# Kernel tuning notes

Measured on AMD Instinct MI355X. Metric: run time of the kernel, lower is better.

## Reference

```python
import jax, jax.numpy as jnp
import numpy as np

N = 1024   # nodes
C = 256    # channels (n_features)
NEG_SLOPE = 0.2


def setup_inputs() -> dict:
    key = jax.random.key(0)
    k1, k2, k3, k4, k5, k6, k7 = jax.random.split(key, 7)
    nodes = jax.random.normal(k1, (N, C), dtype=jnp.float32)
    # dense adjacency used only via (adj != 0); force self-loops so every
    # softmax row has at least one valid entry
    adj_mat = jax.random.randint(k2, (N, N), 0, 2).astype(jnp.int32)
    adj_mat = adj_mat.at[jnp.arange(N), jnp.arange(N)].set(1)
    lim = 1.0 / np.sqrt(C)  # eqx.nn.Linear default uniform init bound
    W_src_w = jax.random.uniform(k3, (C, C), minval=-lim, maxval=lim, dtype=jnp.float32)
    W_src_b = jax.random.uniform(k4, (C,), minval=-lim, maxval=lim, dtype=jnp.float32)
    W_tgt_w = jax.random.uniform(k5, (C, C), minval=-lim, maxval=lim, dtype=jnp.float32)
    W_tgt_b = jax.random.uniform(k6, (C,), minval=-lim, maxval=lim, dtype=jnp.float32)
    a_w = jax.random.uniform(k7, (C,), minval=-lim, maxval=lim, dtype=jnp.float32)  # to_score, no bias
    return {"nodes": nodes, "adj_mat": adj_mat, "W_src_w": W_src_w, "W_src_b": W_src_b,
            "W_tgt_w": W_tgt_w, "W_tgt_b": W_tgt_b, "a_w": a_w}


def reference(nodes, adj_mat, W_src_w, W_src_b, W_tgt_w, W_tgt_b, a_w):
    # per-node linear maps (eqx.nn.Linear: y = W @ x + b)
    g_src = nodes @ W_src_w.T + W_src_b              # [node, C]
    g_tgt = nodes @ W_tgt_w.T + W_tgt_b              # [node, C]
    # g[i, j, c] = g_src[i, c] + g_tgt[j, c]   (axis names as in original: tgt, src)
    g = g_src[:, None, :] + g_tgt[None, :, :]        # [node, node, C]
    g = jax.nn.leaky_relu(g, NEG_SLOPE)
    score = jnp.einsum('ijc,c->ij', g, a_w)          # [node, node]
    score = jnp.where(adj_mat != 0, score, -jnp.inf) # mask non-edges
    weights = jax.nn.softmax(score, axis=1)          # over src axis
    return weights @ g_tgt                           # [node, C]
```

## Files before the change

kernel.cpp:

```cpp
#include <hip/hip_runtime.h>


typedef unsigned short u16;
typedef unsigned int   u32;
typedef _Float16 h2 __attribute__((ext_vector_type(2)));

#define NNODE 1024
#define NC    256
#define NEG   0.2f

__device__ __forceinline__ float bf2f(u16 h) {
    u32 u = ((u32)h) << 16;
    return __builtin_bit_cast(float, u);
}
__device__ __forceinline__ u16 f2bf(float f) {
    u32 u = __builtin_bit_cast(u32, f);
    u32 r = (u + 0x7FFFu + ((u >> 16) & 1u)) >> 16;
    return (u16)r;
}
__device__ __forceinline__ u16 f2h(float f) {
    _Float16 h = (_Float16)f;
    return __builtin_bit_cast(u16, h);
}
__device__ __forceinline__ h2 bch(u32 u) { return __builtin_bit_cast(h2, u); }

__device__ __forceinline__ h2 lrelu2(h2 y) {
    h2 yn = y * (_Float16)NEG;
#if __has_builtin(__builtin_elementwise_max)
    return __builtin_elementwise_max(y, yn);
#else
    h2 r; r.x = y.x > yn.x ? y.x : yn.x; r.y = y.y > yn.y ? y.y : yn.y;
    return r;
#endif
}
__device__ __forceinline__ float dot2(h2 a, h2 b, float acc) {
#if __has_builtin(__builtin_amdgcn_fdot2)
    return __builtin_amdgcn_fdot2(a, b, acc, false);
#else
    acc = fmaf((float)a.x, (float)b.x, acc);
    return fmaf((float)a.y, (float)b.y, acc);
#endif
}

__global__ void detect_kernel(const u16* __restrict__ nodes, int* __restrict__ flag)
{
    const int lane = threadIdx.x;
    ushort4 v = *(const ushort4*)(nodes + lane * 4);
    const u16 h[4] = {v.x, v.y, v.z, v.w};
    int cnt = 0;
    #pragma unroll
    for (int q = 0; q < 4; ++q) {
        int e = (h[q] >> 7) & 0xFF;
        cnt += (e >= 132 || (e >= 1 && e <= 90)) ? 1 : 0;
    }
    #pragma unroll
    for (int off = 32; off; off >>= 1) cnt += __shfl_xor(cnt, off, 64);
    if (lane == 0) *flag = (cnt >= 64) ? 0 : 1;
}

__global__ __launch_bounds__(256) void lin_kernel(
    const void* __restrict__ nodes_v,
    const void* __restrict__ Wsrc_v, const void* __restrict__ bsrc_v,
    const void* __restrict__ Wtgt_v, const void* __restrict__ btgt_v,
    const int* __restrict__ flag,
    u16* __restrict__ gsh, u16* __restrict__ gth)
{
    __shared__ float nT[64][34];
    __shared__ float wT[64][68];

    const int bf = *flag;
    const int t  = threadIdx.x;
    const int ct = blockIdx.x;
    const int it = blockIdx.y;
    const int i0 = it * 32;
    const bool is_src = (ct < 4);
    const int c0 = (is_src ? ct : ct - 4) * 64;
    const void* __restrict__ Wv = is_src ? Wsrc_v : Wtgt_v;
    const void* __restrict__ bv = is_src ? bsrc_v : btgt_v;
    u16* __restrict__ g         = is_src ? gsh : gth;

    const int tc = t & 15, ti = t >> 4;
    float acc[2][4] = {};

    for (int k0 = 0; k0 < NC; k0 += 64) {
        __syncthreads();
        {
            int ii = t & 31, kg = t >> 5;
            float vals[8];
            if (bf) {
                uint4 v = *(const uint4*)((const u16*)nodes_v + (i0 + ii) * NC + k0 + kg * 8);
                const u16* pv = (const u16*)&v;
                #pragma unroll
                for (int q = 0; q < 8; ++q) vals[q] = bf2f(pv[q]);
            } else {
                const float* nf = (const float*)nodes_v;
                float4 v0 = *(const float4*)(nf + (i0 + ii) * NC + k0 + kg * 8);
                float4 v1 = *(const float4*)(nf + (i0 + ii) * NC + k0 + kg * 8 + 4);
                vals[0] = v0.x; vals[1] = v0.y; vals[2] = v0.z; vals[3] = v0.w;
                vals[4] = v1.x; vals[5] = v1.y; vals[6] = v1.z; vals[7] = v1.w;
            }
            #pragma unroll
            for (int q = 0; q < 8; ++q) nT[kg * 8 + q][ii] = vals[q];
        }
        {
            int cc = t & 63, kg = t >> 6;
            float vals[16];
            if (bf) {
                const u16* W = (const u16*)Wv;
                uint4 v0 = *(const uint4*)(W + (c0 + cc) * NC + k0 + kg * 16);
                uint4 v1 = *(const uint4*)(W + (c0 + cc) * NC + k0 + kg * 16 + 8);
                const u16* p0 = (const u16*)&v0;
                const u16* p1 = (const u16*)&v1;
                #pragma unroll
                for (int q = 0; q < 8; ++q) { vals[q] = bf2f(p0[q]); vals[8 + q] = bf2f(p1[q]); }
            } else {
                const float* W = (const float*)Wv;
                #pragma unroll
                for (int h = 0; h < 4; ++h) {
                    float4 v = *(const float4*)(W + (c0 + cc) * NC + k0 + kg * 16 + 4 * h);
                    vals[4 * h + 0] = v.x; vals[4 * h + 1] = v.y;
                    vals[4 * h + 2] = v.z; vals[4 * h + 3] = v.w;
                }
            }
            #pragma unroll
            for (int q = 0; q < 16; ++q) wT[kg * 16 + q][cc] = vals[q];
        }
        __syncthreads();
        #pragma unroll 8
        for (int kk = 0; kk < 64; ++kk) {
            float2 av = *(const float2*)&nT[kk][2 * ti];
            float4 bvv = *(const float4*)&wT[kk][4 * tc];
            float sa[2] = {av.x, av.y};
            float tb[4] = {bvv.x, bvv.y, bvv.z, bvv.w};
            #pragma unroll
            for (int a = 0; a < 2; ++a)
                #pragma unroll
                for (int b = 0; b < 4; ++b)
                    acc[a][b] = fmaf(sa[a], tb[b], acc[a][b]);
        }
    }

    float bb[4];
    #pragma unroll
    for (int q = 0; q < 4; ++q)
        bb[q] = bf ? bf2f(((const u16*)bv)[c0 + 4 * tc + q])
                   : ((const float*)bv)[c0 + 4 * tc + q];
    #pragma unroll
    for (int a = 0; a < 2; ++a) {
        int irow = i0 + 2 * ti + a;
        ushort4 ov;
        ov.x = f2h(acc[a][0] + bb[0]);
        ov.y = f2h(acc[a][1] + bb[1]);
        ov.z = f2h(acc[a][2] + bb[2]);
        ov.w = f2h(acc[a][3] + bb[3]);
        *(ushort4*)(g + (size_t)irow * NC + c0 + 4 * tc) = ov;
    }
}

__global__ __launch_bounds__(256, 4) void fused_kernel(
    const u16* __restrict__ gsh, const u16* __restrict__ gth,
    const void* __restrict__ aw_v, const int* __restrict__ adj,
    const int* __restrict__ flag, int jcnt,
    float* __restrict__ po, float* __restrict__ pm,
    float* __restrict__ pls, void* __restrict__ out_v)
{
    __shared__ u32  gt32[64][132];
    __shared__ u32  gs32[4][128];
    __shared__ u32  a32[128];
    __shared__ float p_lds[4][64];

    const int bf   = *flag;
    const int t    = threadIdx.x;
    const int i    = t >> 6;
    const int lane = t & 63;
    const int row  = blockIdx.x * 4 + i;
    const int z    = blockIdx.y;
    const int jbase = z * jcnt;
    const int jl = lane & 15, q  = lane >> 4;
    const int oc = lane & 31, hh = lane >> 5;

    {
        uint2 v = *(const uint2*)(gsh + (size_t)row * NC + lane * 4);
        *(uint2*)&gs32[i][2 * lane] = v;
    }
    if (t < 128) {
        float a0, a1;
        if (bf) { a0 = bf2f(((const u16*)aw_v)[2 * t]); a1 = bf2f(((const u16*)aw_v)[2 * t + 1]); }
        else    { a0 = ((const float*)aw_v)[2 * t];     a1 = ((const float*)aw_v)[2 * t + 1]; }
        h2 av; av.x = (_Float16)a0; av.y = (_Float16)a1;
        a32[t] = __builtin_bit_cast(u32, av);
    }
    __syncthreads();

    h2 gsr[32];
    #pragma unroll
    for (int k = 0; k < 8; ++k) {
        uint4 gv = *(const uint4*)&gs32[i][q * 32 + 4 * k];
        gsr[4 * k + 0] = bch(gv.x); gsr[4 * k + 1] = bch(gv.y);
        gsr[4 * k + 2] = bch(gv.z); gsr[4 * k + 3] = bch(gv.w);
    }

    float m = -1e30f, l = 0.f;
    float of[8] = {0.f, 0.f, 0.f, 0.f, 0.f, 0.f, 0.f, 0.f};

    for (int j0 = jbase; j0 < jbase + jcnt; j0 += 64) {
        __syncthreads();
        {
            int r = t & 63, seg = t >> 6;
            const u16* src = gth + (size_t)(j0 + r) * NC + seg * 64;
            #pragma unroll
            for (int k = 0; k < 8; ++k) {
                uint4 v = *(const uint4*)(src + 8 * k);
                *(uint4*)&gt32[r][seg * 32 + 4 * k] = v;
            }
        }
        __syncthreads();

        float spv[4] = {0.f, 0.f, 0.f, 0.f};
        #pragma unroll
        for (int k = 0; k < 8; ++k) {
            uint4 a4 = *(const uint4*)&a32[q * 32 + 4 * k];
            h2 a0 = bch(a4.x), a1 = bch(a4.y), a2 = bch(a4.z), a3 = bch(a4.w);
            h2 g0 = gsr[4 * k], g1 = gsr[4 * k + 1],
               g2 = gsr[4 * k + 2], g3 = gsr[4 * k + 3];
            #pragma unroll
            for (int p = 0; p < 4; ++p) {
                uint4 g4 = *(const uint4*)&gt32[16 * p + jl][q * 32 + 4 * k];
                spv[p] = dot2(a0, lrelu2(g0 + bch(g4.x)), spv[p]);
                spv[p] = dot2(a1, lrelu2(g1 + bch(g4.y)), spv[p]);
                spv[p] = dot2(a2, lrelu2(g2 + bch(g4.z)), spv[p]);
                spv[p] = dot2(a3, lrelu2(g3 + bch(g4.w)), spv[p]);
            }
        }
        #pragma unroll
        for (int p = 0; p < 4; ++p) {
            spv[p] += __shfl_xor(spv[p], 16, 64);
            spv[p] += __shfl_xor(spv[p], 32, 64);
        }
        const float s = (lane < 16) ? spv[0] : (lane < 32) ? spv[1]
                      : (lane < 48) ? spv[2] : spv[3];

        const int valid = adj[row * NNODE + j0 + lane];
        float sm = valid ? s : -1e30f;
        float tmax = sm;
        #pragma unroll
        for (int off = 32; off; off >>= 1)
            tmax = fmaxf(tmax, __shfl_xor(tmax, off, 64));
        const float mn    = fmaxf(m, tmax);
        const float alpha = __expf(m - mn);
        const float p     = valid ? __expf(s - mn) : 0.f;
        float ps = p;
        #pragma unroll
        for (int off = 32; off; off >>= 1) ps += __shfl_xor(ps, off, 64);
        l = l * alpha + ps;
        m = mn;
        p_lds[i][lane] = p;

        #pragma unroll
        for (int k = 0; k < 8; ++k) of[k] *= alpha;
        #pragma unroll 8
        for (int jp = 0; jp < 32; ++jp) {
            const float w = p_lds[i][2 * jp + hh];
            uint4 g4 = *(const uint4*)&gt32[2 * jp + hh][4 * oc];
            h2 v0 = bch(g4.x), v1 = bch(g4.y), v2 = bch(g4.z), v3 = bch(g4.w);
            of[0] = fmaf(w, (float)v0.x, of[0]);
            of[1] = fmaf(w, (float)v0.y, of[1]);
            of[2] = fmaf(w, (float)v1.x, of[2]);
            of[3] = fmaf(w, (float)v1.y, of[3]);
            of[4] = fmaf(w, (float)v2.x, of[4]);
            of[5] = fmaf(w, (float)v2.y, of[5]);
            of[6] = fmaf(w, (float)v3.x, of[6]);
            of[7] = fmaf(w, (float)v3.y, of[7]);
        }
    }

    #pragma unroll
    for (int k = 0; k < 8; ++k) of[k] += __shfl_xor(of[k], 32, 64);

    if (lane < 32) {
        if (out_v) {
            const float inv = 1.0f / l;
            if (bf) {
                u16* out = (u16*)out_v;
                ushort4 oa, ob;
                oa.x = f2bf(of[0] * inv); oa.y = f2bf(of[1] * inv);
                oa.z = f2bf(of[2] * inv); oa.w = f2bf(of[3] * inv);
                ob.x = f2bf(of[4] * inv); ob.y = f2bf(of[5] * inv);
                ob.z = f2bf(of[6] * inv); ob.w = f2bf(of[7] * inv);
                *(ushort4*)(out + (size_t)row * NC + 8 * oc)     = oa;
                *(ushort4*)(out + (size_t)row * NC + 8 * oc + 4) = ob;
            } else {
                float* out = (float*)out_v;
                *(float4*)(out + (size_t)row * NC + 8 * oc) =
                    make_float4(of[0] * inv, of[1] * inv, of[2] * inv, of[3] * inv);
                *(float4*)(out + (size_t)row * NC + 8 * oc + 4) =
                    make_float4(of[4] * inv, of[5] * inv, of[6] * inv, of[7] * inv);
            }
        } else {
            float* pp = po + ((size_t)z * NNODE + row) * NC + 8 * oc;
            *(float4*)pp       = make_float4(of[0], of[1], of[2], of[3]);
            *(float4*)(pp + 4) = make_float4(of[4], of[5], of[6], of[7]);
        }
    }
    if (!out_v && lane == 0) {
        pm [z * NNODE + row] = m;
        pls[z * NNODE + row] = l;
    }
}

__global__ __launch_bounds__(256) void combine_kernel(
    const float* __restrict__ po, const float* __restrict__ pm,
    const float* __restrict__ pls, const int* __restrict__ flag,
    int ns, void* __restrict__ out_v)
{
    const int bf  = *flag;
    const int row = blockIdx.x;
    const int c   = threadIdx.x;

    float mstar = -1e30f;
    for (int zz = 0; zz < ns; ++zz)
        mstar = fmaxf(mstar, pm[zz * NNODE + row]);

    float acc = 0.f, lsum = 0.f;
    for (int zz = 0; zz < ns; ++zz) {
        const float wz = __expf(pm[zz * NNODE + row] - mstar);
        lsum = fmaf(pls[zz * NNODE + row], wz, lsum);
        acc  = fmaf(po[(size_t)(zz * NNODE + row) * NC + c], wz, acc);
    }
    const float v = acc / lsum;
    if (bf) ((u16*)out_v)[row * NC + c] = f2bf(v);
    else    ((float*)out_v)[row * NC + c] = v;
}

extern "C" void kernel_launch(void* const* d_in, const int* in_sizes, int n_in,
                              void* d_out, int out_size, void* d_ws, size_t ws_size,
                              hipStream_t stream)
{
    const int* adj = (const int*)d_in[1];

    char* wsb = (char*)d_ws;
    int* flag = (int*)wsb;
    u16* gsh  = (u16*)(wsb + 256);
    u16* gth  = gsh + (size_t)NNODE * NC;

    detect_kernel<<<1, 64, 0, stream>>>((const u16*)d_in[0], flag);
    lin_kernel<<<dim3(8, 32), 256, 0, stream>>>(d_in[0], d_in[2], d_in[3],
                                                d_in[4], d_in[5], flag, gsh, gth);

    const size_t base = 256 + 2ull * NNODE * NC * sizeof(u16);
    int NS = 0;
    {
        size_t need4 = base + (4ull * NNODE * NC + 8ull * NNODE) * 4ull;
        size_t need2 = base + (2ull * NNODE * NC + 4ull * NNODE) * 4ull;
        if      (ws_size >= need4) NS = 4;
        else if (ws_size >= need2) NS = 2;
    }

    if (NS) {
        float* po  = (float*)(wsb + base);
        float* pm  = po + (size_t)NS * NNODE * NC;
        float* pls = pm + (size_t)NS * NNODE;
        fused_kernel<<<dim3(256, NS), 256, 0, stream>>>(
            gsh, gth, d_in[6], adj, flag, NNODE / NS, po, pm, pls, nullptr);
        combine_kernel<<<NNODE, 256, 0, stream>>>(po, pm, pls, flag, NS, d_out);
    } else {
        fused_kernel<<<dim3(256, 1), 256, 0, stream>>>(
            gsh, gth, d_in[6], adj, flag, NNODE, nullptr, nullptr, nullptr, d_out);
    }
}
```

Measured before the change: 68.44 us.

## Process two target rows per wave, swizzle LDS tile, inline dtype detection

Each wave now handles two output rows, so every g_tgt tile value read from LDS feeds two score and aggregation computations, doubling reuse and halving the number of blocks. The LDS tile drops its padding in favour of an XOR swizzle to avoid bank conflicts. The separate detect kernel is removed and each kernel detects the dtype itself, saving a launch. The split count can rise to 8 when workspace allows. The cost is higher register pressure from the doubled accumulators and g_src registers, and a larger combine step.

```diff
diff --git a/kernel.cpp b/kernel.cpp
--- a/kernel.cpp
+++ b/kernel.cpp
@@ -42,9 +42,8 @@
 #endif
 }
 
-__global__ void detect_kernel(const u16* __restrict__ nodes, int* __restrict__ flag)
-{
-    const int lane = threadIdx.x;
+__device__ __forceinline__ int wave_detect(const u16* __restrict__ nodes, int lane)
+{
     ushort4 v = *(const ushort4*)(nodes + lane * 4);
     const u16 h[4] = {v.x, v.y, v.z, v.w};
     int cnt = 0;
@@ -55,21 +54,22 @@
     }
     #pragma unroll
     for (int off = 32; off; off >>= 1) cnt += __shfl_xor(cnt, off, 64);
-    if (lane == 0) *flag = (cnt >= 64) ? 0 : 1;
-}
+    return (cnt >= 64) ? 0 : 1;
+}
+
+__device__ __forceinline__ int swz(int grp, int row) { return grp ^ (row & 31); }
 
 __global__ __launch_bounds__(256) void lin_kernel(
     const void* __restrict__ nodes_v,
     const void* __restrict__ Wsrc_v, const void* __restrict__ bsrc_v,
     const void* __restrict__ Wtgt_v, const void* __restrict__ btgt_v,
-    const int* __restrict__ flag,
     u16* __restrict__ gsh, u16* __restrict__ gth)
 {
     __shared__ float nT[64][34];
     __shared__ float wT[64][68];
 
-    const int bf = *flag;
     const int t  = threadIdx.x;
+    const int bf = wave_detect((const u16*)nodes_v, t & 63);
     const int ct = blockIdx.x;
     const int it = blockIdx.y;
     const int i0 = it * 32;
@@ -160,29 +160,24 @@
 __global__ __launch_bounds__(256, 4) void fused_kernel(
     const u16* __restrict__ gsh, const u16* __restrict__ gth,
     const void* __restrict__ aw_v, const int* __restrict__ adj,
-    const int* __restrict__ flag, int jcnt,
+    const u16* __restrict__ nodes_u16, int jcnt,
     float* __restrict__ po, float* __restrict__ pm,
     float* __restrict__ pls, void* __restrict__ out_v)
 {
-    __shared__ u32  gt32[64][132];
-    __shared__ u32  gs32[4][128];
-    __shared__ u32  a32[128];
-    __shared__ float p_lds[4][64];
-
-    const int bf   = *flag;
+    __shared__ u32   gt32[64 * 128];
+    __shared__ u32   a32[128];
+    __shared__ float p_lds[8][64];
+
     const int t    = threadIdx.x;
-    const int i    = t >> 6;
+    const int wv   = t >> 6;
     const int lane = t & 63;
-    const int row  = blockIdx.x * 4 + i;
+    const int bf   = wave_detect(nodes_u16, lane);
+    const int r0   = blockIdx.x * 8 + 2 * wv;
     const int z    = blockIdx.y;
     const int jbase = z * jcnt;
     const int jl = lane & 15, q  = lane >> 4;
     const int oc = lane & 31, hh = lane >> 5;
 
-    {
-        uint2 v = *(const uint2*)(gsh + (size_t)row * NC + lane * 4);
-        *(uint2*)&gs32[i][2 * lane] = v;
-    }
     if (t < 128) {
         float a0, a1;
         if (bf) { a0 = bf2f(((const u16*)aw_v)[2 * t]); a1 = bf2f(((const u16*)aw_v)[2 * t + 1]); }
@@ -190,130 +185,167 @@
         h2 av; av.x = (_Float16)a0; av.y = (_Float16)a1;
         a32[t] = __builtin_bit_cast(u32, av);
     }
-    __syncthreads();
-
-    h2 gsr[32];
-    #pragma unroll
-    for (int k = 0; k < 8; ++k) {
-        uint4 gv = *(const uint4*)&gs32[i][q * 32 + 4 * k];
-        gsr[4 * k + 0] = bch(gv.x); gsr[4 * k + 1] = bch(gv.y);
-        gsr[4 * k + 2] = bch(gv.z); gsr[4 * k + 3] = bch(gv.w);
-    }
-
-    float m = -1e30f, l = 0.f;
-    float of[8] = {0.f, 0.f, 0.f, 0.f, 0.f, 0.f, 0.f, 0.f};
+
+    u32 gsr[2][32];
+    #pragma unroll
+    for (int r = 0; r < 2; ++r) {
+        const u16* src = gsh + (size_t)(r0 + r) * NC + q * 64;
+        #pragma unroll
+        for (int k = 0; k < 8; ++k) {
+            uint4 gv = *(const uint4*)(src + 8 * k);
+            gsr[r][4 * k + 0] = gv.x; gsr[r][4 * k + 1] = gv.y;
+            gsr[r][4 * k + 2] = gv.z; gsr[r][4 * k + 3] = gv.w;
+        }
+    }
+
+    float m[2] = {-1e30f, -1e30f}, l[2] = {0.f, 0.f};
+    float of[2][8] = {};
 
     for (int j0 = jbase; j0 < jbase + jcnt; j0 += 64) {
         __syncthreads();
         {
-            int r = t & 63, seg = t >> 6;
-            const u16* src = gth + (size_t)(j0 + r) * NC + seg * 64;
+            int rr = t & 63, seg = t >> 6;
+            const u16* src = gth + (size_t)(j0 + rr) * NC + seg * 64;
+            u32* dst = gt32 + rr * 128;
             #pragma unroll
             for (int k = 0; k < 8; ++k) {
                 uint4 v = *(const uint4*)(src + 8 * k);
-                *(uint4*)&gt32[r][seg * 32 + 4 * k] = v;
+                *(uint4*)(dst + swz(seg * 8 + k, rr) * 4) = v;
             }
         }
         __syncthreads();
 
-        float spv[4] = {0.f, 0.f, 0.f, 0.f};
+        float spv[2][4] = {};
         #pragma unroll
         for (int k = 0; k < 8; ++k) {
             uint4 a4 = *(const uint4*)&a32[q * 32 + 4 * k];
             h2 a0 = bch(a4.x), a1 = bch(a4.y), a2 = bch(a4.z), a3 = bch(a4.w);
-            h2 g0 = gsr[4 * k], g1 = gsr[4 * k + 1],
-               g2 = gsr[4 * k + 2], g3 = gsr[4 * k + 3];
             #pragma unroll
             for (int p = 0; p < 4; ++p) {
-                uint4 g4 = *(const uint4*)&gt32[16 * p + jl][q * 32 + 4 * k];
-                spv[p] = dot2(a0, lrelu2(g0 + bch(g4.x)), spv[p]);
-                spv[p] = dot2(a1, lrelu2(g1 + bch(g4.y)), spv[p]);
-                spv[p] = dot2(a2, lrelu2(g2 + bch(g4.z)), spv[p]);
-                spv[p] = dot2(a3, lrelu2(g3 + bch(g4.w)), spv[p]);
-            }
-        }
-        #pragma unroll
-        for (int p = 0; p < 4; ++p) {
-            spv[p] += __shfl_xor(spv[p], 16, 64);
-            spv[p] += __shfl_xor(spv[p], 32, 64);
-        }
-        const float s = (lane < 16) ? spv[0] : (lane < 32) ? spv[1]
-                      : (lane < 48) ? spv[2] : spv[3];
-
-        const int valid = adj[row * NNODE + j0 + lane];
-        float sm = valid ? s : -1e30f;
-        float tmax = sm;
-        #pragma unroll
-        for (int off = 32; off; off >>= 1)
-            tmax = fmaxf(tmax, __shfl_xor(tmax, off, 64));
-        const float mn    = fmaxf(m, tmax);
-        const float alpha = __expf(m - mn);
-        const float p     = valid ? __expf(s - mn) : 0.f;
-        float ps = p;
-        #pragma unroll
-        for (int off = 32; off; off >>= 1) ps += __shfl_xor(ps, off, 64);
-        l = l * alpha + ps;
-        m = mn;
-        p_lds[i][lane] = p;
-
-        #pragma unroll
-        for (int k = 0; k < 8; ++k) of[k] *= alpha;
-        #pragma unroll 8
+                const int rowp = 16 * p + jl;
+                uint4 g4 = *(const uint4*)&gt32[rowp * 128 + swz(q * 8 + k, rowp) * 4];
+                h2 t0 = bch(g4.x), t1 = bch(g4.y), t2 = bch(g4.z), t3 = bch(g4.w);
+                #pragma unroll
+                for (int r = 0; r < 2; ++r) {
+                    spv[r][p] = dot2(a0, lrelu2(bch(gsr[r][4 * k + 0]) + t0), spv[r][p]);
+                    spv[r][p] = dot2(a1, lrelu2(bch(gsr[r][4 * k + 1]) + t1), spv[r][p]);
+                    spv[r][p] = dot2(a2, lrelu2(bch(gsr[r][4 * k + 2]) + t2), spv[r][p]);
+                    spv[r][p] = dot2(a3, lrelu2(bch(gsr[r][4 * k + 3]) + t3), spv[r][p]);
+                }
+            }
+        }
+        #pragma unroll
+        for (int r = 0; r < 2; ++r)
+            #pragma unroll
+            for (int p = 0; p < 4; ++p) {
+                spv[r][p] += __shfl_xor(spv[r][p], 16, 64);
+                spv[r][p] += __shfl_xor(spv[r][p], 32, 64);
+            }
+
+        float alpha[2];
+        #pragma unroll
+        for (int r = 0; r < 2; ++r) {
+            const float s = (lane < 16) ? spv[r][0] : (lane < 32) ? spv[r][1]
+                          : (lane < 48) ? spv[r][2] : spv[r][3];
+            const int valid = adj[(size_t)(r0 + r) * NNODE + j0 + lane];
+            float sm = valid ? s : -1e30f;
+            float tmax = sm;
+            #pragma unroll
+            for (int off = 32; off; off >>= 1)
+                tmax = fmaxf(tmax, __shfl_xor(tmax, off, 64));
+            const float mn = fmaxf(m[r], tmax);
+            alpha[r]       = __expf(m[r] - mn);
+            const float p  = valid ? __expf(s - mn) : 0.f;
+            float ps = p;
+            #pragma unroll
+            for (int off = 32; off; off >>= 1) ps += __shfl_xor(ps, off, 64);
+            l[r] = l[r] * alpha[r] + ps;
+            m[r] = mn;
+            p_lds[2 * wv + r][lane] = p;
+        }
+
+        #pragma unroll
+        for (int r = 0; r < 2; ++r)
+            #pragma unroll
+            for (int k = 0; k < 8; ++k) of[r][k] *= alpha[r];
+
+        #pragma unroll 4
         for (int jp = 0; jp < 32; ++jp) {
-            const float w = p_lds[i][2 * jp + hh];
-            uint4 g4 = *(const uint4*)&gt32[2 * jp + hh][4 * oc];
+            const int j = 2 * jp + hh;
+            const float w0 = p_lds[2 * wv    ][j];
+            const float w1 = p_lds[2 * wv + 1][j];
+            uint4 g4 = *(const uint4*)&gt32[j * 128 + swz(oc, j) * 4];
             h2 v0 = bch(g4.x), v1 = bch(g4.y), v2 = bch(g4.z), v3 = bch(g4.w);
-            of[0] = fmaf(w, (float)v0.x, of[0]);
-            of[1] = fmaf(w, (float)v0.y, of[1]);
-            of[2] = fmaf(w, (float)v1.x, of[2]);
-            of[3] = fmaf(w, (float)v1.y, of[3]);
-            of[4] = fmaf(w, (float)v2.x, of[4]);
-            of[5] = fmaf(w, (float)v2.y, of[5]);
-            of[6] = fmaf(w, (float)v3.x, of[6]);
-            of[7] = fmaf(w, (float)v3.y, of[7]);
-        }
-    }
-
-    #pragma unroll
-    for (int k = 0; k < 8; ++k) of[k] += __shfl_xor(of[k], 32, 64);
+            of[0][0] = fmaf(w0, (float)v0.x, of[0][0]);
+            of[0][1] = fmaf(w0, (float)v0.y, of[0][1]);
+            of[0][2] = fmaf(w0, (float)v1.x, of[0][2]);
+            of[0][3] = fmaf(w0, (float)v1.y, of[0][3]);
+            of[0][4] = fmaf(w0, (float)v2.x, of[0][4]);
+            of[0][5] = fmaf(w0, (float)v2.y, of[0][5]);
+            of[0][6] = fmaf(w0, (float)v3.x, of[0][6]);
+            of[0][7] = fmaf(w0, (float)v3.y, of[0][7]);
+            of[1][0] = fmaf(w1, (float)v0.x, of[1][0]);
+            of[1][1] = fmaf(w1, (float)v0.y, of[1][1]);
+            of[1][2] = fmaf(w1, (float)v1.x, of[1][2]);
+            of[1][3] = fmaf(w1, (float)v1.y, of[1][3]);
+            of[1][4] = fmaf(w1, (float)v2.x, of[1][4]);
+            of[1][5] = fmaf(w1, (float)v2.y, of[1][5]);
+            of[1][6] = fmaf(w1, (float)v3.x, of[1][6]);
+            of[1][7] = fmaf(w1, (float)v3.y, of[1][7]);
+        }
+    }
+
+    #pragma unroll
+    for (int r = 0; r < 2; ++r)
+        #pragma unroll
+        for (int k = 0; k < 8; ++k) of[r][k] += __shfl_xor(of[r][k], 32, 64);
 
     if (lane < 32) {
-        if (out_v) {
-            const float inv = 1.0f / l;
-            if (bf) {
-                u16* out = (u16*)out_v;
-                ushort4 oa, ob;
-                oa.x = f2bf(of[0] * inv); oa.y = f2bf(of[1] * inv);
-                oa.z = f2bf(of[2] * inv); oa.w = f2bf(of[3] * inv);
-                ob.x = f2bf(of[4] * inv); ob.y = f2bf(of[5] * inv);
-                ob.z = f2bf(of[6] * inv); ob.w = f2bf(of[7] * inv);
-                *(ushort4*)(out + (size_t)row * NC + 8 * oc)     = oa;
-                *(ushort4*)(out + (size_t)row * NC + 8 * oc + 4) = ob;
+        #pragma unroll
+        for (int r = 0; r < 2; ++r) {
+            const int row = r0 + r;
+            if (out_v) {
+                const float inv = 1.0f / l[r];
+                if (bf) {
+                    u16* out = (u16*)out_v;
+                    ushort4 oa, ob;
+                    oa.x = f2bf(of[r][0] * inv); oa.y = f2bf(of[r][1] * inv);
+                    oa.z = f2bf(of[r][2] * inv); oa.w = f2bf(of[r][3] * inv);
+                    ob.x = f2bf(of[r][4] * inv); ob.y = f2bf(of[r][5] * inv);
+                    ob.z = f2bf(of[r][6] * inv); ob.w = f2bf(of[r][7] * inv);
+                    *(ushort4*)(out + (size_t)row * NC + 8 * oc)     = oa;
+                    *(ushort4*)(out + (size_t)row * NC + 8 * oc + 4) = ob;
+                } else {
+                    float* out = (float*)out_v;
+                    *(float4*)(out + (size_t)row * NC + 8 * oc) =
+                        make_float4(of[r][0] * inv, of[r][1] * inv,
+                                    of[r][2] * inv, of[r][3] * inv);
+                    *(float4*)(out + (size_t)row * NC + 8 * oc + 4) =
+                        make_float4(of[r][4] * inv, of[r][5] * inv,
+                                    of[r][6] * inv, of[r][7] * inv);
+                }
             } else {
-                float* out = (float*)out_v;
-                *(float4*)(out + (size_t)row * NC + 8 * oc) =
-                    make_float4(of[0] * inv, of[1] * inv, of[2] * inv, of[3] * inv);
-                *(float4*)(out + (size_t)row * NC + 8 * oc + 4) =
-                    make_float4(of[4] * inv, of[5] * inv, of[6] * inv, of[7] * inv);
-            }
-        } else {
-            float* pp = po + ((size_t)z * NNODE + row) * NC + 8 * oc;
-            *(float4*)pp       = make_float4(of[0], of[1], of[2], of[3]);
-            *(float4*)(pp + 4) = make_float4(of[4], of[5], of[6], of[7]);
+                float* pp = po + ((size_t)z * NNODE + row) * NC + 8 * oc;
+                *(float4*)pp       = make_float4(of[r][0], of[r][1], of[r][2], of[r][3]);
+                *(float4*)(pp + 4) = make_float4(of[r][4], of[r][5], of[r][6], of[r][7]);
+            }
         }
     }
     if (!out_v && lane == 0) {
-        pm [z * NNODE + row] = m;
-        pls[z * NNODE + row] = l;
+        #pragma unroll
+        for (int r = 0; r < 2; ++r) {
+            pm [(size_t)z * NNODE + r0 + r] = m[r];
+            pls[(size_t)z * NNODE + r0 + r] = l[r];
+        }
     }
 }
 
 __global__ __launch_bounds__(256) void combine_kernel(
     const float* __restrict__ po, const float* __restrict__ pm,
-    const float* __restrict__ pls, const int* __restrict__ flag,
+    const float* __restrict__ pls, const u16* __restrict__ nodes_u16,
     int ns, void* __restrict__ out_v)
 {
-    const int bf  = *flag;
+    const int bf  = wave_detect(nodes_u16, threadIdx.x & 63);
     const int row = blockIdx.x;
     const int c   = threadIdx.x;
 
@@ -336,35 +368,32 @@
                               void* d_out, int out_size, void* d_ws, size_t ws_size,
                               hipStream_t stream)
 {
-    const int* adj = (const int*)d_in[1];
+    const u16* nodes_u16 = (const u16*)d_in[0];
+    const int* adj       = (const int*)d_in[1];
 
     char* wsb = (char*)d_ws;
-    int* flag = (int*)wsb;
-    u16* gsh  = (u16*)(wsb + 256);
+    u16* gsh  = (u16*)wsb;
     u16* gth  = gsh + (size_t)NNODE * NC;
 
-    detect_kernel<<<1, 64, 0, stream>>>((const u16*)d_in[0], flag);
     lin_kernel<<<dim3(8, 32), 256, 0, stream>>>(d_in[0], d_in[2], d_in[3],
-                                                d_in[4], d_in[5], flag, gsh, gth);
-
-    const size_t base = 256 + 2ull * NNODE * NC * sizeof(u16);
+                                                d_in[4], d_in[5], gsh, gth);
+
+    const size_t base = 2ull * NNODE * NC * sizeof(u16);
+    const size_t per  = 4ull * NNODE * NC + 8ull * NNODE;
     int NS = 0;
-    {
-        size_t need4 = base + (4ull * NNODE * NC + 8ull * NNODE) * 4ull;
-        size_t need2 = base + (2ull * NNODE * NC + 4ull * NNODE) * 4ull;
-        if      (ws_size >= need4) NS = 4;
-        else if (ws_size >= need2) NS = 2;
-    }
+    if      (ws_size >= base + 8 * per) NS = 8;
+    else if (ws_size >= base + 4 * per) NS = 4;
+    else if (ws_size >= base + 2 * per) NS = 2;
 
     if (NS) {
         float* po  = (float*)(wsb + base);
         float* pm  = po + (size_t)NS * NNODE * NC;
         float* pls = pm + (size_t)NS * NNODE;
-        fused_kernel<<<dim3(256, NS), 256, 0, stream>>>(
-            gsh, gth, d_in[6], adj, flag, NNODE / NS, po, pm, pls, nullptr);
-        combine_kernel<<<NNODE, 256, 0, stream>>>(po, pm, pls, flag, NS, d_out);
+        fused_kernel<<<dim3(128, NS), 256, 0, stream>>>(
+            gsh, gth, d_in[6], adj, nodes_u16, NNODE / NS, po, pm, pls, nullptr);
+        combine_kernel<<<NNODE, 256, 0, stream>>>(po, pm, pls, nodes_u16, NS, d_out);
     } else {
-        fused_kernel<<<dim3(256, 1), 256, 0, stream>>>(
-            gsh, gth, d_in[6], adj, flag, NNODE, nullptr, nullptr, nullptr, d_out);
-    }
-}
+        fused_kernel<<<dim3(128, 1), 256, 0, stream>>>(
+            gsh, gth, d_in[6], adj, nodes_u16, NNODE, nullptr, nullptr, nullptr, d_out);
+    }
+}
```

Result: slower. 72.13 us (+5.4%).

## Rewrite leaky ReLU as linear plus abs term and precompute linear score parts

Applied to the files above, without the earlier changes.

Uses leaky_relu(x) = 0.6x + 0.4|x|, so the per-pair inner loop only computes an abs (a bit mask) instead of a multiply and max. The linear parts become per-row and per-column dot products: one is computed in a new sdot kernel, the other inside the fused kernel. The change also removes the detect kernel by recomputing the dtype flag in every wave, XOR-swizzles the shared-memory tile instead of padding it, loads gsrc straight into registers, and allows an 8-way split over the source axis. Costs are an extra launch, a larger partial buffer for combine, and different fp16 rounding in the score.

```diff
diff --git a/kernel.cpp b/kernel.cpp
--- a/kernel.cpp
+++ b/kernel.cpp
@@ -23,15 +23,9 @@
     return __builtin_bit_cast(u16, h);
 }
 __device__ __forceinline__ h2 bch(u32 u) { return __builtin_bit_cast(h2, u); }
-
-__device__ __forceinline__ h2 lrelu2(h2 y) {
-    h2 yn = y * (_Float16)NEG;
-#if __has_builtin(__builtin_elementwise_max)
-    return __builtin_elementwise_max(y, yn);
-#else
-    h2 r; r.x = y.x > yn.x ? y.x : yn.x; r.y = y.y > yn.y ? y.y : yn.y;
-    return r;
-#endif
+__device__ __forceinline__ h2 habs2(h2 y) {
+    u32 u = __builtin_bit_cast(u32, y) & 0x7FFF7FFFu;
+    return __builtin_bit_cast(h2, u);
 }
 __device__ __forceinline__ float dot2(h2 a, h2 b, float acc) {
 #if __has_builtin(__builtin_amdgcn_fdot2)
@@ -42,9 +36,8 @@
 #endif
 }
 
-__global__ void detect_kernel(const u16* __restrict__ nodes, int* __restrict__ flag)
-{
-    const int lane = threadIdx.x;
+__device__ __forceinline__ int wave_detect(const u16* __restrict__ nodes, int lane)
+{
     ushort4 v = *(const ushort4*)(nodes + lane * 4);
     const u16 h[4] = {v.x, v.y, v.z, v.w};
     int cnt = 0;
@@ -55,21 +48,22 @@
     }
     #pragma unroll
     for (int off = 32; off; off >>= 1) cnt += __shfl_xor(cnt, off, 64);
-    if (lane == 0) *flag = (cnt >= 64) ? 0 : 1;
-}
+    return (cnt >= 64) ? 0 : 1;
+}
+
+__device__ __forceinline__ int swz(int grp, int row) { return grp ^ (row & 31); }
 
 __global__ __launch_bounds__(256) void lin_kernel(
     const void* __restrict__ nodes_v,
     const void* __restrict__ Wsrc_v, const void* __restrict__ bsrc_v,
     const void* __restrict__ Wtgt_v, const void* __restrict__ btgt_v,
-    const int* __restrict__ flag,
     u16* __restrict__ gsh, u16* __restrict__ gth)
 {
     __shared__ float nT[64][34];
     __shared__ float wT[64][68];
 
-    const int bf = *flag;
     const int t  = threadIdx.x;
+    const int bf = wave_detect((const u16*)nodes_v, t & 63);
     const int ct = blockIdx.x;
     const int it = blockIdx.y;
     const int i0 = it * 32;
@@ -157,79 +151,124 @@
     }
 }
 
+__global__ __launch_bounds__(256) void sdot_kernel(
+    const u16* __restrict__ gth, const void* __restrict__ aw_v,
+    const u16* __restrict__ nodes_u16, float* __restrict__ sgt06)
+{
+    const int t    = threadIdx.x;
+    const int lane = t & 63;
+    const int bf   = wave_detect(nodes_u16, lane);
+    const int row  = blockIdx.x * 4 + (t >> 6);
+
+    float a0, a1, a2, a3;
+    if (bf) {
+        ushort4 a4 = *(const ushort4*)((const u16*)aw_v + lane * 4);
+        a0 = bf2f(a4.x); a1 = bf2f(a4.y); a2 = bf2f(a4.z); a3 = bf2f(a4.w);
+    } else {
+        float4 a4 = *(const float4*)((const float*)aw_v + lane * 4);
+        a0 = a4.x; a1 = a4.y; a2 = a4.z; a3 = a4.w;
+    }
+    ushort4 gv = *(const ushort4*)(gth + (size_t)row * NC + lane * 4);
+    float s = a0 * (float)__builtin_bit_cast(_Float16, gv.x)
+            + a1 * (float)__builtin_bit_cast(_Float16, gv.y)
+            + a2 * (float)__builtin_bit_cast(_Float16, gv.z)
+            + a3 * (float)__builtin_bit_cast(_Float16, gv.w);
+    #pragma unroll
+    for (int off = 32; off; off >>= 1) s += __shfl_xor(s, off, 64);
+    if (lane == 0) sgt06[row] = 0.6f * s;
+}
+
 __global__ __launch_bounds__(256, 4) void fused_kernel(
     const u16* __restrict__ gsh, const u16* __restrict__ gth,
     const void* __restrict__ aw_v, const int* __restrict__ adj,
-    const int* __restrict__ flag, int jcnt,
-    float* __restrict__ po, float* __restrict__ pm,
+    const u16* __restrict__ nodes_u16, const float* __restrict__ sgt06,
+    int jcnt, float* __restrict__ po, float* __restrict__ pm,
     float* __restrict__ pls, void* __restrict__ out_v)
 {
-    __shared__ u32  gt32[64][132];
-    __shared__ u32  gs32[4][128];
-    __shared__ u32  a32[128];
+    __shared__ u32   gt32[64 * 128];
+    __shared__ u32   a32[128];
     __shared__ float p_lds[4][64];
 
-    const int bf   = *flag;
     const int t    = threadIdx.x;
     const int i    = t >> 6;
     const int lane = t & 63;
+    const int bf   = wave_detect(nodes_u16, lane);
     const int row  = blockIdx.x * 4 + i;
     const int z    = blockIdx.y;
     const int jbase = z * jcnt;
     const int jl = lane & 15, q  = lane >> 4;
     const int oc = lane & 31, hh = lane >> 5;
 
-    {
-        uint2 v = *(const uint2*)(gsh + (size_t)row * NC + lane * 4);
-        *(uint2*)&gs32[i][2 * lane] = v;
-    }
     if (t < 128) {
         float a0, a1;
         if (bf) { a0 = bf2f(((const u16*)aw_v)[2 * t]); a1 = bf2f(((const u16*)aw_v)[2 * t + 1]); }
         else    { a0 = ((const float*)aw_v)[2 * t];     a1 = ((const float*)aw_v)[2 * t + 1]; }
-        h2 av; av.x = (_Float16)a0; av.y = (_Float16)a1;
+        h2 av; av.x = (_Float16)(0.4f * a0); av.y = (_Float16)(0.4f * a1);
         a32[t] = __builtin_bit_cast(u32, av);
     }
+
+    u32 gsr[32];
+    {
+        const u16* src = gsh + (size_t)row * NC + q * 64;
+        #pragma unroll
+        for (int k = 0; k < 8; ++k) {
+            uint4 gv = *(const uint4*)(src + 8 * k);
+            gsr[4 * k + 0] = gv.x; gsr[4 * k + 1] = gv.y;
+            gsr[4 * k + 2] = gv.z; gsr[4 * k + 3] = gv.w;
+        }
+    }
     __syncthreads();
 
-    h2 gsr[32];
-    #pragma unroll
-    for (int k = 0; k < 8; ++k) {
-        uint4 gv = *(const uint4*)&gs32[i][q * 32 + 4 * k];
-        gsr[4 * k + 0] = bch(gv.x); gsr[4 * k + 1] = bch(gv.y);
-        gsr[4 * k + 2] = bch(gv.z); gsr[4 * k + 3] = bch(gv.w);
+    float Sgs06;
+    {
+        float sg = 0.f;
+        #pragma unroll
+        for (int k = 0; k < 8; ++k) {
+            uint4 a4 = *(const uint4*)&a32[q * 32 + 4 * k];
+            sg = dot2(bch(a4.x), bch(gsr[4 * k + 0]), sg);
+            sg = dot2(bch(a4.y), bch(gsr[4 * k + 1]), sg);
+            sg = dot2(bch(a4.z), bch(gsr[4 * k + 2]), sg);
+            sg = dot2(bch(a4.w), bch(gsr[4 * k + 3]), sg);
+        }
+        sg += __shfl_xor(sg, 16, 64);
+        sg += __shfl_xor(sg, 32, 64);
+        Sgs06 = 1.5f * sg;
     }
 
     float m = -1e30f, l = 0.f;
-    float of[8] = {0.f, 0.f, 0.f, 0.f, 0.f, 0.f, 0.f, 0.f};
+    float of[8] = {};
 
     for (int j0 = jbase; j0 < jbase + jcnt; j0 += 64) {
         __syncthreads();
         {
-            int r = t & 63, seg = t >> 6;
-            const u16* src = gth + (size_t)(j0 + r) * NC + seg * 64;
+            int rr = t & 63, seg = t >> 6;
+            const u16* src = gth + (size_t)(j0 + rr) * NC + seg * 64;
+            u32* dst = gt32 + rr * 128;
             #pragma unroll
             for (int k = 0; k < 8; ++k) {
                 uint4 v = *(const uint4*)(src + 8 * k);
-                *(uint4*)&gt32[r][seg * 32 + 4 * k] = v;
+                *(uint4*)(dst + swz(seg * 8 + k, rr) * 4) = v;
             }
         }
         __syncthreads();
 
-        float spv[4] = {0.f, 0.f, 0.f, 0.f};
+        const float sgtj = sgt06[j0 + lane];
+
+        float spv[4] = {};
         #pragma unroll
         for (int k = 0; k < 8; ++k) {
             uint4 a4 = *(const uint4*)&a32[q * 32 + 4 * k];
             h2 a0 = bch(a4.x), a1 = bch(a4.y), a2 = bch(a4.z), a3 = bch(a4.w);
-            h2 g0 = gsr[4 * k], g1 = gsr[4 * k + 1],
-               g2 = gsr[4 * k + 2], g3 = gsr[4 * k + 3];
+            h2 g0 = bch(gsr[4 * k + 0]), g1 = bch(gsr[4 * k + 1]),
+               g2 = bch(gsr[4 * k + 2]), g3 = bch(gsr[4 * k + 3]);
             #pragma unroll
             for (int p = 0; p < 4; ++p) {
-                uint4 g4 = *(const uint4*)&gt32[16 * p + jl][q * 32 + 4 * k];
-                spv[p] = dot2(a0, lrelu2(g0 + bch(g4.x)), spv[p]);
-                spv[p] = dot2(a1, lrelu2(g1 + bch(g4.y)), spv[p]);
-                spv[p] = dot2(a2, lrelu2(g2 + bch(g4.z)), spv[p]);
-                spv[p] = dot2(a3, lrelu2(g3 + bch(g4.w)), spv[p]);
+                const int rowp = 16 * p + jl;
+                uint4 g4 = *(const uint4*)&gt32[rowp * 128 + swz(q * 8 + k, rowp) * 4];
+                spv[p] = dot2(a0, habs2(g0 + bch(g4.x)), spv[p]);
+                spv[p] = dot2(a1, habs2(g1 + bch(g4.y)), spv[p]);
+                spv[p] = dot2(a2, habs2(g2 + bch(g4.z)), spv[p]);
+                spv[p] = dot2(a3, habs2(g3 + bch(g4.w)), spv[p]);
             }
         }
         #pragma unroll
@@ -237,10 +276,11 @@
             spv[p] += __shfl_xor(spv[p], 16, 64);
             spv[p] += __shfl_xor(spv[p], 32, 64);
         }
-        const float s = (lane < 16) ? spv[0] : (lane < 32) ? spv[1]
-                      : (lane < 48) ? spv[2] : spv[3];
-
-        const int valid = adj[row * NNODE + j0 + lane];
+        const float sabs = (lane < 16) ? spv[0] : (lane < 32) ? spv[1]
+                         : (lane < 48) ? spv[2] : spv[3];
+        const float s = sabs + Sgs06 + sgtj;
+
+        const int valid = adj[(size_t)row * NNODE + j0 + lane];
         float sm = valid ? s : -1e30f;
         float tmax = sm;
         #pragma unroll
@@ -260,8 +300,9 @@
         for (int k = 0; k < 8; ++k) of[k] *= alpha;
         #pragma unroll 8
         for (int jp = 0; jp < 32; ++jp) {
-            const float w = p_lds[i][2 * jp + hh];
-            uint4 g4 = *(const uint4*)&gt32[2 * jp + hh][4 * oc];
+            const int j = 2 * jp + hh;
+            const float w = p_lds[i][j];
+            uint4 g4 = *(const uint4*)&gt32[j * 128 + swz(oc, j) * 4];
             h2 v0 = bch(g4.x), v1 = bch(g4.y), v2 = bch(g4.z), v3 = bch(g4.w);
             of[0] = fmaf(w, (float)v0.x, of[0]);
             of[1] = fmaf(w, (float)v0.y, of[1]);
@@ -303,17 +344,17 @@
         }
     }
     if (!out_v && lane == 0) {
-        pm [z * NNODE + row] = m;
-        pls[z * NNODE + row] = l;
+        pm [(size_t)z * NNODE + row] = m;
+        pls[(size_t)z * NNODE + row] = l;
     }
 }
 
 __global__ __launch_bounds__(256) void combine_kernel(
     const float* __restrict__ po, const float* __restrict__ pm,
-    const float* __restrict__ pls, const int* __restrict__ flag,
+    const float* __restrict__ pls, const u16* __restrict__ nodes_u16,
     int ns, void* __restrict__ out_v)
 {
-    const int bf  = *flag;
+    const int bf  = wave_detect(nodes_u16, threadIdx.x & 63);
     const int row = blockIdx.x;
     const int c   = threadIdx.x;
 
@@ -336,35 +377,36 @@
                               void* d_out, int out_size, void* d_ws, size_t ws_size,
                               hipStream_t stream)
 {
-    const int* adj = (const int*)d_in[1];
-
-    char* wsb = (char*)d_ws;
-    int* flag = (int*)wsb;
-    u16* gsh  = (u16*)(wsb + 256);
-    u16* gth  = gsh + (size_t)NNODE * NC;
-
-    detect_kernel<<<1, 64, 0, stream>>>((const u16*)d_in[0], flag);
+    const u16* nodes_u16 = (const u16*)d_in[0];
+    const int* adj       = (const int*)d_in[1];
+
+    char*  wsb   = (char*)d_ws;
+    u16*   gsh   = (u16*)wsb;
+    u16*   gth   = gsh + (size_t)NNODE * NC;
+    float* sgt06 = (float*)(wsb + 2ull * NNODE * NC * sizeof(u16));
+
     lin_kernel<<<dim3(8, 32), 256, 0, stream>>>(d_in[0], d_in[2], d_in[3],
-                                                d_in[4], d_in[5], flag, gsh, gth);
-
-    const size_t base = 256 + 2ull * NNODE * NC * sizeof(u16);
+                                                d_in[4], d_in[5], gsh, gth);
+    sdot_kernel<<<256, 256, 0, stream>>>(gth, d_in[6], nodes_u16, sgt06);
+
+    const size_t base = 2ull * NNODE * NC * sizeof(u16) + NNODE * sizeof(float);
+    const size_t per  = 4ull * NNODE * NC + 8ull * NNODE;
     int NS = 0;
-    {
-        size_t need4 = base + (4ull * NNODE * NC + 8ull * NNODE) * 4ull;
-        size_t need2 = base + (2ull * NNODE * NC + 4ull * NNODE) * 4ull;
-        if      (ws_size >= need4) NS = 4;
-        else if (ws_size >= need2) NS = 2;
-    }
+    if      (ws_size >= base + 8 * per) NS = 8;
+    else if (ws_size >= base + 4 * per) NS = 4;
+    else if (ws_size >= base + 2 * per) NS = 2;
 
     if (NS) {
         float* po  = (float*)(wsb + base);
         float* pm  = po + (size_t)NS * NNODE * NC;
         float* pls = pm + (size_t)NS * NNODE;
         fused_kernel<<<dim3(256, NS), 256, 0, stream>>>(
-            gsh, gth, d_in[6], adj, flag, NNODE / NS, po, pm, pls, nullptr);
-        combine_kernel<<<NNODE, 256, 0, stream>>>(po, pm, pls, flag, NS, d_out);
+            gsh, gth, d_in[6], adj, nodes_u16, sgt06, NNODE / NS,
+            po, pm, pls, nullptr);
+        combine_kernel<<<NNODE, 256, 0, stream>>>(po, pm, pls, nodes_u16, NS, d_out);
     } else {
         fused_kernel<<<dim3(256, 1), 256, 0, stream>>>(
-            gsh, gth, d_in[6], adj, flag, NNODE, nullptr, nullptr, nullptr, d_out);
-    }
-}
+            gsh, gth, d_in[6], adj, nodes_u16, sgt06, NNODE,
+            nullptr, nullptr, nullptr, d_out);
+    }
+}
```

New measurement: 70.16 us. 2.5% more time.
